# Performance work log

Hardware: AMD Instinct MI355X
Metric: run time of the kernel (lower is better)

Reference implementation:

```python
import jax, jax.numpy as jnp
import numpy as np

NUM_HEADS = 12


def setup_inputs() -> dict:
    key = jax.random.key(0)
    k1, k2, k3, k4, k5 = jax.random.split(key, 5)
    B, H, W, C = 8, 32, 32, 768
    x = jax.random.normal(k1, (B, H, W, C), dtype=jnp.float32)
    # torch nn.Linear weights: (out_features, in_features)
    qkv_w = jax.random.normal(k2, (3 * C, C), dtype=jnp.float32) * (C ** -0.5)
    qkv_b = jax.random.normal(k3, (3 * C,), dtype=jnp.float32) * 0.02
    proj_w = jax.random.normal(k4, (C, C), dtype=jnp.float32) * (C ** -0.5)
    proj_b = jax.random.normal(k5, (C,), dtype=jnp.float32) * 0.02
    return {"x": x, "qkv_w": qkv_w, "qkv_b": qkv_b, "proj_w": proj_w, "proj_b": proj_b}


def reference(x, qkv_w, qkv_b, proj_w, proj_b):
    B, H, W, C = x.shape
    nh = NUM_HEADS
    hd = C // nh
    scale = hd ** -0.5
    L = H * W
    # qkv projection: (B, L, 3C)
    qkv = jnp.einsum('bhwc,oc->bhwo', x, qkv_w) + qkv_b
    # -> (3, B*nh, L, hd)
    qkv = qkv.reshape(B, L, 3, nh, hd).transpose(2, 0, 3, 1, 4).reshape(3, B * nh, L, hd)
    q, k, v = qkv[0], qkv[1], qkv[2]
    # attention scores (B*nh, L, L)
    attn = jnp.einsum('bqd,bkd->bqk', q * scale, k)
    attn = jax.nn.softmax(attn, axis=-1)
    out = jnp.einsum('bqk,bkd->bqd', attn, v)  # (B*nh, L, hd)
    out = out.reshape(B, nh, H, W, hd).transpose(0, 2, 3, 1, 4).reshape(B, H, W, C)
    out = jnp.einsum('bhwc,oc->bhwo', out, proj_w) + proj_b
    return out
```

## Files before the change

### kernel.cpp

```cpp
#include <hip/hip_runtime.h>


typedef __attribute__((ext_vector_type(8))) __bf16 bf16x8;
typedef __attribute__((ext_vector_type(4))) __bf16 bf16x4;
typedef __attribute__((ext_vector_type(4))) float f32x4;

#define GLL16(g, l) __builtin_amdgcn_global_load_lds( \
    (const __attribute__((address_space(1))) void*)(g), \
    (__attribute__((address_space(3))) void*)(l), 16, 0, 0)

static __device__ __forceinline__ f32x4 mfma16(bf16x8 a, bf16x8 b, f32x4 c) {
  return __builtin_amdgcn_mfma_f32_16x16x32_bf16(a, b, c, 0, 0, 0);
}

static __device__ __forceinline__ float exp2_hw(float x) {
  return __builtin_amdgcn_exp2f(x);
}

static __device__ __forceinline__ int swz64(int row, int col) {
  return (row * 64 + col) ^ ((row & 7) << 3);
}

__global__ __launch_bounds__(256) void cvt_all(const float* __restrict__ x,
                                               const float* __restrict__ wq,
                                               const float* __restrict__ wp,
                                               __bf16* __restrict__ dst,
                                               int nx4, int nwq4, int total4) {
  const int i = blockIdx.x * 256 + threadIdx.x;
  if (i >= total4) return;
  const float* src;
  int off;
  if (i < nx4) { src = x; off = i; }
  else if (i < nx4 + nwq4) { src = wq; off = i - nx4; }
  else { src = wp; off = i - nx4 - nwq4; }
  const float4 v = *(const float4*)&src[(size_t)off * 4];
  bf16x4 o;
  o[0] = (__bf16)v.x; o[1] = (__bf16)v.y; o[2] = (__bf16)v.z; o[3] = (__bf16)v.w;
  *(bf16x4*)&dst[(size_t)i * 4] = o;
}

template <int EPI>
__global__ __launch_bounds__(256) void gemm_nt(const __bf16* __restrict__ A,
                                               const __bf16* __restrict__ Bw,
                                               const float* __restrict__ bias,
                                               float* __restrict__ out,
                                               __bf16* __restrict__ Qb,
                                               __bf16* __restrict__ Kb,
                                               __bf16* __restrict__ Vtb,
                                               int M, int N, int K) {
  __shared__ alignas(16) __bf16 smem[3 * 4096 * 2];
  const int tid = threadIdx.x;
  const int lane = tid & 63;
  const int wave = tid >> 6;
  const int wr = wave >> 1, wc = wave & 1;
  const int l15 = lane & 15, lhi = lane >> 4;
  const int mbase = blockIdx.x * 128;
  const int nbase = blockIdx.y * 128;

  f32x4 acc[4][4];
#pragma unroll
  for (int m = 0; m < 4; ++m)
#pragma unroll
    for (int n = 0; n < 4; ++n) acc[m][n] = (f32x4){0.f, 0.f, 0.f, 0.f};

  const int e0 = wave * 512 + lane * 8;
  const int e1 = e0 + 2048;
  const int ar0 = mbase + (e0 >> 5), ac0 = e0 & 31;
  const int ar1 = mbase + (e1 >> 5), ac1 = e1 & 31;
  const int br0 = nbase + (e0 >> 5);
  const int br1 = nbase + (e1 >> 5);

  const int nkt = K >> 5;

#define STAGE(t, bf) do { \
    const int kb_ = (t) << 5; \
    GLL16(A + (size_t)ar0 * K + kb_ + ac0, &smem[(bf) * 4096 + e0]); \
    GLL16(A + (size_t)ar1 * K + kb_ + ac1, &smem[(bf) * 4096 + e1]); \
    GLL16(Bw + (size_t)br0 * K + kb_ + ac0, &smem[12288 + (bf) * 4096 + e0]); \
    GLL16(Bw + (size_t)br1 * K + kb_ + ac1, &smem[12288 + (bf) * 4096 + e1]); \
  } while (0)

  STAGE(0, 0);
  STAGE(1, 1);

  int cur = 0, nx2 = 2;
  for (int kt = 0; kt < nkt; ++kt) {
    if (kt + 1 < nkt)
      asm volatile("s_waitcnt vmcnt(4)" ::: "memory");
    else
      asm volatile("s_waitcnt vmcnt(0)" ::: "memory");
    __builtin_amdgcn_s_barrier();
    asm volatile("" ::: "memory");
    if (kt + 2 < nkt) STAGE(kt + 2, nx2);

    const __bf16* bufA = &smem[cur * 4096];
    const __bf16* bufB = &smem[12288 + cur * 4096];
    bf16x8 a[4], b[4];
#pragma unroll
    for (int m = 0; m < 4; ++m)
      a[m] = *(const bf16x8*)&bufA[(wr * 64 + m * 16 + l15) * 32 + lhi * 8];
#pragma unroll
    for (int n = 0; n < 4; ++n)
      b[n] = *(const bf16x8*)&bufB[(wc * 64 + n * 16 + l15) * 32 + lhi * 8];
#pragma unroll
    for (int m = 0; m < 4; ++m)
#pragma unroll
      for (int n = 0; n < 4; ++n)
        acc[m][n] = mfma16(a[m], b[n], acc[m][n]);

    cur = (cur == 2) ? 0 : cur + 1;
    nx2 = (nx2 == 2) ? 0 : nx2 + 1;
  }
#undef STAGE

  if (EPI == 0 && nbase >= 1536) {
    __syncthreads();
    __bf16* ldsT = &smem[0];
#pragma unroll
    for (int n = 0; n < 4; ++n) {
      const int gl = wc * 64 + n * 16 + l15;
      const float bv = bias[nbase + gl];
#pragma unroll
      for (int m = 0; m < 4; ++m) {
        bf16x4 pk;
#pragma unroll
        for (int i = 0; i < 4; ++i) pk[i] = (__bf16)(acc[m][n][i] + bv);
        *(bf16x4*)&ldsT[gl * 136 + wr * 64 + m * 16 + lhi * 4] = pk;
      }
    }
    __syncthreads();
    const int r = tid >> 1;
    const int half = tid & 1;
    const int head = ((nbase - 1536) >> 6) + (r >> 6);
    const int d = r & 63;
    const int bb = mbase >> 10;
    const int lbase = mbase & 1023;
    __bf16* dst = Vtb + ((size_t)(bb * 12 + head) * 64 + d) * 1024 + lbase + half * 64;
    const __bf16* srcl = &ldsT[r * 136 + half * 64];
#pragma unroll
    for (int j = 0; j < 8; ++j)
      *(bf16x8*)&dst[j * 8] = *(const bf16x8*)&srcl[j * 8];
    return;
  }

#pragma unroll
  for (int n = 0; n < 4; ++n) {
    const int gcol = nbase + wc * 64 + n * 16 + l15;
    const float bv = bias[gcol];
    if (EPI == 1) {
#pragma unroll
      for (int m = 0; m < 4; ++m)
#pragma unroll
        for (int i = 0; i < 4; ++i) {
          const int grow = mbase + wr * 64 + m * 16 + lhi * 4 + i;
          out[(size_t)grow * N + gcol] = acc[m][n][i] + bv;
        }
    } else {
      const int three = gcol / 768;
      const int rem = gcol - three * 768;
      const int head = rem >> 6;
      const int d = rem & 63;
#pragma unroll
      for (int m = 0; m < 4; ++m)
#pragma unroll
        for (int i = 0; i < 4; ++i) {
          const int grow = mbase + wr * 64 + m * 16 + lhi * 4 + i;
          const int bb = grow >> 10;
          const int lrow = grow & 1023;
          const int bh = bb * 12 + head;
          const float v = acc[m][n][i] + bv;
          if (three == 0)
            Qb[((size_t)bh * 1024 + lrow) * 64 + d] = (__bf16)(v * 0.18033688f);
          else
            Kb[((size_t)bh * 1024 + lrow) * 64 + d] = (__bf16)v;
        }
    }
  }
}

__global__ __launch_bounds__(512, 6) void attn_fwd(const __bf16* __restrict__ Q,
                                                   const __bf16* __restrict__ Kg,
                                                   const __bf16* __restrict__ Vt,
                                                   __bf16* __restrict__ O) {
  __shared__ alignas(16) __bf16 lK[2][64 * 64];
  __shared__ alignas(16) __bf16 lV[2][64 * 64];
  __shared__ alignas(16) __bf16 lP[8][16 * 72];
  const int tid = threadIdx.x, lane = tid & 63, wave = tid >> 6;
  const int l15 = lane & 15, lhi = lane >> 4;
  const int bh = blockIdx.x, qt = blockIdx.y;
  const int b = bh / 12, head = bh % 12;

  bf16x8 q[2];
  {
    const int qrow = qt * 128 + wave * 16 + l15;
#pragma unroll
    for (int kk = 0; kk < 2; ++kk)
      q[kk] = *(const bf16x8*)&Q[((size_t)bh * 1024 + qrow) * 64 + kk * 32 + lhi * 8];
  }

  f32x4 o[4];
  float mrun = -3.0e38f, lrun = 0.f;
#pragma unroll
  for (int n = 0; n < 4; ++n) o[n] = (f32x4){0.f, 0.f, 0.f, 0.f};

  const int q0b = tid * 16;
  const int p0b = q0b ^ (((q0b >> 7) & 7) << 4);
  const int e0 = q0b >> 1;
  const int kofs0 = p0b >> 1;
  const int vofs0 = (p0b >> 7) * 1024 + ((p0b & 127) >> 1);

  const __bf16* kbase = Kg + (size_t)bh * 1024 * 64;
  const __bf16* vbase = Vt + (size_t)bh * 64 * 1024;

  GLL16(kbase + kofs0, &lK[0][e0]);
  GLL16(vbase + vofs0, &lV[0][e0]);
  __syncthreads();

  for (int kv = 0; kv < 16; ++kv) {
    const int cur = kv & 1;
    if (kv + 1 < 16) {
      GLL16(kbase + (kv + 1) * 4096 + kofs0, &lK[cur ^ 1][e0]);
      GLL16(vbase + (kv + 1) * 64 + vofs0, &lV[cur ^ 1][e0]);
    }

    f32x4 s[4];
#pragma unroll
    for (int km = 0; km < 4; ++km) {
      bf16x8 k0 = *(const bf16x8*)&lK[cur][swz64(km * 16 + l15, lhi * 8)];
      bf16x8 k1 = *(const bf16x8*)&lK[cur][swz64(km * 16 + l15, 32 + lhi * 8)];
      f32x4 z = (f32x4){0.f, 0.f, 0.f, 0.f};
      z = mfma16(k0, q[0], z);
      z = mfma16(k1, q[1], z);
      s[km] = z;
    }

    float lm = s[0][0];
#pragma unroll
    for (int km = 0; km < 4; ++km)
#pragma unroll
      for (int i = 0; i < 4; ++i) lm = fmaxf(lm, s[km][i]);

    if (!__all(lm - mrun <= 8.f)) {
      float r = lm;
      r = fmaxf(r, __shfl_xor(r, 16));
      r = fmaxf(r, __shfl_xor(r, 32));
      const float mnew = fmaxf(mrun, r);
      const float alpha = exp2_hw(mrun - mnew);
      mrun = mnew;
      lrun *= alpha;
      float am[4];
#pragma unroll
      for (int i = 0; i < 4; ++i) am[i] = __shfl(alpha, (lhi << 2) | i, 64);
#pragma unroll
      for (int n = 0; n < 4; ++n)
#pragma unroll
        for (int i = 0; i < 4; ++i) o[n][i] *= am[i];
    }

    {
      float ps = 0.f;
#pragma unroll
      for (int km = 0; km < 4; ++km) {
        bf16x4 pk;
#pragma unroll
        for (int i = 0; i < 4; ++i) {
          const float p = exp2_hw(s[km][i] - mrun);
          ps += p;
          pk[i] = (__bf16)p;
        }
        *(bf16x4*)&lP[wave][l15 * 72 + km * 16 + lhi * 4] = pk;
      }
      lrun += ps;
    }

    bf16x8 vf[4][2];
#pragma unroll
    for (int n = 0; n < 4; ++n)
#pragma unroll
      for (int kk = 0; kk < 2; ++kk)
        vf[n][kk] = *(const bf16x8*)&lV[cur][swz64(n * 16 + l15, kk * 32 + lhi * 8)];
    {
      bf16x8 p0 = *(const bf16x8*)&lP[wave][l15 * 72 + lhi * 8];
      bf16x8 p1 = *(const bf16x8*)&lP[wave][l15 * 72 + 32 + lhi * 8];
#pragma unroll
      for (int n = 0; n < 4; ++n) {
        o[n] = mfma16(p0, vf[n][0], o[n]);
        o[n] = mfma16(p1, vf[n][1], o[n]);
      }
    }
    __syncthreads();
  }

  float r = lrun;
  r += __shfl_xor(r, 16);
  r += __shfl_xor(r, 32);
  const float inv = 1.f / r;
  float im[4];
#pragma unroll
  for (int i = 0; i < 4; ++i) im[i] = __shfl(inv, (lhi << 2) | i, 64);
#pragma unroll
  for (int i = 0; i < 4; ++i) {
    const int lrow = qt * 128 + wave * 16 + lhi * 4 + i;
#pragma unroll
    for (int n = 0; n < 4; ++n) {
      const int col = head * 64 + n * 16 + l15;
      O[((size_t)b * 1024 + lrow) * 768 + col] = (__bf16)(o[n][i] * im[i]);
    }
  }
}

extern "C" void kernel_launch(void* const* d_in, const int* in_sizes, int n_in,
                              void* d_out, int out_size, void* d_ws, size_t ws_size,
                              hipStream_t stream) {
  const float* x = (const float*)d_in[0];
  const float* qkv_w = (const float*)d_in[1];
  const float* qkv_b = (const float*)d_in[2];
  const float* proj_w = (const float*)d_in[3];
  const float* proj_b = (const float*)d_in[4];
  float* out = (float*)d_out;

  const size_t NX = (size_t)8192 * 768;
  const size_t NWQ = (size_t)2304 * 768;
  const size_t NWP = (size_t)768 * 768;
  const size_t SZ = (size_t)96 * 1024 * 64;

  __bf16* xb = (__bf16*)d_ws;
  __bf16* wqkvb = xb + NX;
  __bf16* wprojb = wqkvb + NWQ;
  __bf16* Q = wprojb + NWP;
  __bf16* K = Q + SZ;
  __bf16* Vt = K + SZ;
  __bf16* AO = Vt + SZ;

  const int nx4 = (int)(NX / 4), nwq4 = (int)(NWQ / 4), nwp4 = (int)(NWP / 4);
  const int total4 = nx4 + nwq4 + nwp4;
  cvt_all<<<(total4 + 255) / 256, 256, 0, stream>>>(x, qkv_w, proj_w, xb, nx4, nwq4, total4);

  gemm_nt<0><<<dim3(64, 18), 256, 0, stream>>>(xb, wqkvb, qkv_b, nullptr, Q, K, Vt,
                                               8192, 2304, 768);
  attn_fwd<<<dim3(96, 8), 512, 0, stream>>>(Q, K, Vt, AO);
  gemm_nt<1><<<dim3(64, 6), 256, 0, stream>>>(AO, wprojb, proj_b, out,
                                              nullptr, nullptr, nullptr, 8192, 768, 768);
}
```

Before: 116.1 us.

## Enlarge GEMM tile to 256x128 with each wave owning 64 rows

The QKV and output-projection GEMMs now use 256x128 block tiles instead of 128x128. Each of the four waves computes a 64x128 strip, which raises MFMA work per LDS load and halves the number of blocks. The V-transpose epilogue is split into two LDS passes so it fits the existing buffer. The cost is a 4x8 accumulator array, which raises register pressure, and fewer blocks: 192 for the projection GEMM on a GPU with many CUs, so occupancy and wave quantization may get worse.

Measured after the change: 119.3 us. 1.03x slower.

```diff
diff --git a/kernel.cpp b/kernel.cpp
--- a/kernel.cpp
+++ b/kernel.cpp
@@ -40,44 +40,42 @@
 }
 
 template <int EPI>
-__global__ __launch_bounds__(256) void gemm_nt(const __bf16* __restrict__ A,
-                                               const __bf16* __restrict__ Bw,
-                                               const float* __restrict__ bias,
-                                               float* __restrict__ out,
-                                               __bf16* __restrict__ Qb,
-                                               __bf16* __restrict__ Kb,
-                                               __bf16* __restrict__ Vtb,
-                                               int M, int N, int K) {
-  __shared__ alignas(16) __bf16 smem[3 * 4096 * 2];
+__global__ __launch_bounds__(256, 2) void gemm_nt(const __bf16* __restrict__ A,
+                                                  const __bf16* __restrict__ Bw,
+                                                  const float* __restrict__ bias,
+                                                  float* __restrict__ out,
+                                                  __bf16* __restrict__ Qb,
+                                                  __bf16* __restrict__ Kb,
+                                                  __bf16* __restrict__ Vtb,
+                                                  int M, int N, int K) {
+  __shared__ alignas(16) __bf16 smem[24576 + 12288];
   const int tid = threadIdx.x;
   const int lane = tid & 63;
   const int wave = tid >> 6;
-  const int wr = wave >> 1, wc = wave & 1;
   const int l15 = lane & 15, lhi = lane >> 4;
-  const int mbase = blockIdx.x * 128;
+  const int mbase = blockIdx.x * 256;
   const int nbase = blockIdx.y * 128;
 
-  f32x4 acc[4][4];
+  f32x4 acc[4][8];
 #pragma unroll
   for (int m = 0; m < 4; ++m)
 #pragma unroll
-    for (int n = 0; n < 4; ++n) acc[m][n] = (f32x4){0.f, 0.f, 0.f, 0.f};
-
-  const int e0 = wave * 512 + lane * 8;
-  const int e1 = e0 + 2048;
-  const int ar0 = mbase + (e0 >> 5), ac0 = e0 & 31;
-  const int ar1 = mbase + (e1 >> 5), ac1 = e1 & 31;
-  const int br0 = nbase + (e0 >> 5);
-  const int br1 = nbase + (e1 >> 5);
+    for (int n = 0; n < 8; ++n) acc[m][n] = (f32x4){0.f, 0.f, 0.f, 0.f};
+
+  const int e0 = tid * 8;
+  const int crow = tid >> 2;
+  const int ccol = (tid & 3) * 8;
 
   const int nkt = K >> 5;
 
 #define STAGE(t, bf) do { \
     const int kb_ = (t) << 5; \
-    GLL16(A + (size_t)ar0 * K + kb_ + ac0, &smem[(bf) * 4096 + e0]); \
-    GLL16(A + (size_t)ar1 * K + kb_ + ac1, &smem[(bf) * 4096 + e1]); \
-    GLL16(Bw + (size_t)br0 * K + kb_ + ac0, &smem[12288 + (bf) * 4096 + e0]); \
-    GLL16(Bw + (size_t)br1 * K + kb_ + ac1, &smem[12288 + (bf) * 4096 + e1]); \
+    GLL16(A + (size_t)(mbase + 0 * 64 + crow) * K + kb_ + ccol, &smem[(bf) * 8192 + 0 * 2048 + e0]); \
+    GLL16(A + (size_t)(mbase + 1 * 64 + crow) * K + kb_ + ccol, &smem[(bf) * 8192 + 1 * 2048 + e0]); \
+    GLL16(A + (size_t)(mbase + 2 * 64 + crow) * K + kb_ + ccol, &smem[(bf) * 8192 + 2 * 2048 + e0]); \
+    GLL16(A + (size_t)(mbase + 3 * 64 + crow) * K + kb_ + ccol, &smem[(bf) * 8192 + 3 * 2048 + e0]); \
+    GLL16(Bw + (size_t)(nbase + 0 * 64 + crow) * K + kb_ + ccol, &smem[24576 + (bf) * 4096 + 0 * 2048 + e0]); \
+    GLL16(Bw + (size_t)(nbase + 1 * 64 + crow) * K + kb_ + ccol, &smem[24576 + (bf) * 4096 + 1 * 2048 + e0]); \
   } while (0)
 
   STAGE(0, 0);
@@ -86,26 +84,26 @@
   int cur = 0, nx2 = 2;
   for (int kt = 0; kt < nkt; ++kt) {
     if (kt + 1 < nkt)
-      asm volatile("s_waitcnt vmcnt(4)" ::: "memory");
+      asm volatile("s_waitcnt vmcnt(6)" ::: "memory");
     else
       asm volatile("s_waitcnt vmcnt(0)" ::: "memory");
     __builtin_amdgcn_s_barrier();
     asm volatile("" ::: "memory");
     if (kt + 2 < nkt) STAGE(kt + 2, nx2);
 
-    const __bf16* bufA = &smem[cur * 4096];
-    const __bf16* bufB = &smem[12288 + cur * 4096];
-    bf16x8 a[4], b[4];
+    const __bf16* bufA = &smem[cur * 8192];
+    const __bf16* bufB = &smem[24576 + cur * 4096];
+    bf16x8 a[4], b[8];
 #pragma unroll
     for (int m = 0; m < 4; ++m)
-      a[m] = *(const bf16x8*)&bufA[(wr * 64 + m * 16 + l15) * 32 + lhi * 8];
-#pragma unroll
-    for (int n = 0; n < 4; ++n)
-      b[n] = *(const bf16x8*)&bufB[(wc * 64 + n * 16 + l15) * 32 + lhi * 8];
+      a[m] = *(const bf16x8*)&bufA[(wave * 64 + m * 16 + l15) * 32 + lhi * 8];
+#pragma unroll
+    for (int n = 0; n < 8; ++n)
+      b[n] = *(const bf16x8*)&bufB[(n * 16 + l15) * 32 + lhi * 8];
 #pragma unroll
     for (int m = 0; m < 4; ++m)
 #pragma unroll
-      for (int n = 0; n < 4; ++n)
+      for (int n = 0; n < 8; ++n)
         acc[m][n] = mfma16(a[m], b[n], acc[m][n]);
 
     cur = (cur == 2) ? 0 : cur + 1;
@@ -114,45 +112,51 @@
 #undef STAGE
 
   if (EPI == 0 && nbase >= 1536) {
-    __syncthreads();
     __bf16* ldsT = &smem[0];
-#pragma unroll
-    for (int n = 0; n < 4; ++n) {
-      const int gl = wc * 64 + n * 16 + l15;
-      const float bv = bias[nbase + gl];
-#pragma unroll
-      for (int m = 0; m < 4; ++m) {
-        bf16x4 pk;
-#pragma unroll
-        for (int i = 0; i < 4; ++i) pk[i] = (__bf16)(acc[m][n][i] + bv);
-        *(bf16x4*)&ldsT[gl * 136 + wr * 64 + m * 16 + lhi * 4] = pk;
-      }
-    }
-    __syncthreads();
+    const int bb = mbase >> 10;
+    const int lbase = mbase & 1023;
     const int r = tid >> 1;
     const int half = tid & 1;
     const int head = ((nbase - 1536) >> 6) + (r >> 6);
     const int d = r & 63;
-    const int bb = mbase >> 10;
-    const int lbase = mbase & 1023;
-    __bf16* dst = Vtb + ((size_t)(bb * 12 + head) * 64 + d) * 1024 + lbase + half * 64;
-    const __bf16* srcl = &ldsT[r * 136 + half * 64];
-#pragma unroll
-    for (int j = 0; j < 8; ++j)
-      *(bf16x8*)&dst[j * 8] = *(const bf16x8*)&srcl[j * 8];
+#pragma unroll
+    for (int h = 0; h < 2; ++h) {
+      __syncthreads();
+      if ((wave >> 1) == h) {
+        const int rloc = (wave & 1) * 64;
+#pragma unroll
+        for (int n = 0; n < 8; ++n) {
+          const int gl = n * 16 + l15;
+          const float bv = bias[nbase + gl];
+#pragma unroll
+          for (int m = 0; m < 4; ++m) {
+            bf16x4 pk;
+#pragma unroll
+            for (int i = 0; i < 4; ++i) pk[i] = (__bf16)(acc[m][n][i] + bv);
+            *(bf16x4*)&ldsT[gl * 136 + rloc + m * 16 + lhi * 4] = pk;
+          }
+        }
+      }
+      __syncthreads();
+      __bf16* dst = Vtb + ((size_t)(bb * 12 + head) * 64 + d) * 1024 + lbase + h * 128 + half * 64;
+      const __bf16* srcl = &ldsT[r * 136 + half * 64];
+#pragma unroll
+      for (int j = 0; j < 8; ++j)
+        *(bf16x8*)&dst[j * 8] = *(const bf16x8*)&srcl[j * 8];
+    }
     return;
   }
 
 #pragma unroll
-  for (int n = 0; n < 4; ++n) {
-    const int gcol = nbase + wc * 64 + n * 16 + l15;
+  for (int n = 0; n < 8; ++n) {
+    const int gcol = nbase + n * 16 + l15;
     const float bv = bias[gcol];
     if (EPI == 1) {
 #pragma unroll
       for (int m = 0; m < 4; ++m)
 #pragma unroll
         for (int i = 0; i < 4; ++i) {
-          const int grow = mbase + wr * 64 + m * 16 + lhi * 4 + i;
+          const int grow = mbase + wave * 64 + m * 16 + lhi * 4 + i;
           out[(size_t)grow * N + gcol] = acc[m][n][i] + bv;
         }
     } else {
@@ -164,7 +168,7 @@
       for (int m = 0; m < 4; ++m)
 #pragma unroll
         for (int i = 0; i < 4; ++i) {
-          const int grow = mbase + wr * 64 + m * 16 + lhi * 4 + i;
+          const int grow = mbase + wave * 64 + m * 16 + lhi * 4 + i;
           const int bb = grow >> 10;
           const int lrow = grow & 1023;
           const int bh = bb * 12 + head;
@@ -336,9 +340,9 @@
   const int total4 = nx4 + nwq4 + nwp4;
   cvt_all<<<(total4 + 255) / 256, 256, 0, stream>>>(x, qkv_w, proj_w, xb, nx4, nwq4, total4);
 
-  gemm_nt<0><<<dim3(64, 18), 256, 0, stream>>>(xb, wqkvb, qkv_b, nullptr, Q, K, Vt,
+  gemm_nt<0><<<dim3(32, 18), 256, 0, stream>>>(xb, wqkvb, qkv_b, nullptr, Q, K, Vt,
                                                8192, 2304, 768);
   attn_fwd<<<dim3(96, 8), 512, 0, stream>>>(Q, K, Vt, AO);
-  gemm_nt<1><<<dim3(64, 6), 256, 0, stream>>>(AO, wprojb, proj_b, out,
+  gemm_nt<1><<<dim3(32, 6), 256, 0, stream>>>(AO, wprojb, proj_b, out,
                                               nullptr, nullptr, nullptr, 8192, 768, 768);
 }
```
